# Kernel tuning notes

Measured on AMD Instinct MI355X. Metric: run time of the kernel, lower is better.

The kernel has to match this reference:

```python
import jax, jax.numpy as jnp
import numpy as np

IN_SIZE = 224
KERNEL = 5
STRIDE = 1
IN_CH = 16
OUT_CH = 64
LAMB = 5.0
LR = 0.005
GAMMA = 0.99
EPS_ = 0.01
NH = (IN_SIZE - KERNEL) // STRIDE + 1          # 220 output positions per side
NB_TILES = NH * NH                              # 48400 tiles


def setup_inputs() -> dict:
    key = jax.random.key(0)
    k1, k2 = jax.random.split(key)
    x = jax.random.normal(k1, (1, IN_CH, IN_SIZE, IN_SIZE), dtype=jnp.float32)
    # torch.nn.init.uniform_(param, a=0, b=1)
    W = jax.random.uniform(k2, (OUT_CH, IN_CH, KERNEL, KERNEL), dtype=jnp.float32)
    exp_avg = jnp.zeros((OUT_CH,), dtype=jnp.float32)
    return {"x": x, "W": W, "exp_avg": exp_avg, "clamped": 0}


def _inhibition(out):
    out = jax.nn.relu(out)
    m = jnp.max(out, axis=1, keepdims=True)     # max over channel dim
    out = out / (m + 1e-9)
    return out ** LAMB


def _flatten_input(x):
    # mirrors x.unfold(2,k,s).unfold(3,k,s) -> [T, C*k*k] with (C, kh, kw) ordering
    starts = jnp.arange(NH) * STRIDE
    rows = starts[:, None] + jnp.arange(KERNEL)  # [NH, K]
    p = x[0][:, rows]                            # [C, NH, K, W]
    p = p[:, :, :, rows]                         # [C, NH, K, NH, K]
    p = p.transpose(1, 3, 0, 2, 4)               # [NH, NH, C, K, K]
    return p.reshape(NB_TILES, -1)               # [T, D]


def reference(x, W, exp_avg, clamped):
    # forward conv + inhibition
    out = jax.lax.conv_general_dilated(
        x, W, (STRIDE, STRIDE), 'VALID',
        dimension_numbers=('NCHW', 'OIHW', 'NCHW'))
    out = _inhibition(out)                       # [1, O, NH, NH]

    # Hebbian FullyOrthogonal update (no-grad buffer update in the original)
    y = out[0].transpose(1, 2, 0).reshape(-1, OUT_CH)   # [T, O]
    xf = _flatten_input(x)                               # [T, D]
    Wf = W.reshape(OUT_CH, -1)                           # [O, D]
    # mean_t( lr * (y_t (x) x_t - y_t (x) (y_t W)) ) = lr/T * (Y^T X - (Y^T Y) W)
    yty = y.T @ y                                        # [O, O]
    avg_delta = (LR / NB_TILES) * (y.T @ xf - yty @ Wf)  # [O, D]
    Wnew = jax.nn.relu(Wf + avg_delta).reshape(OUT_CH, IN_CH, KERNEL, KERNEL)
    exp_new = GAMMA * exp_avg + (1.0 - GAMMA) * jnp.mean(y, axis=0)

    # weight decay scaling
    A = exp_new / jnp.mean(exp_new)
    gfp = EPS_ * jnp.tanh(-EPS_ * (A - 1.0)) + 1.0
    gfn = 1.0 / gfp
    pos = jnp.where(Wnew > 0, Wnew, 0.0) * gfp.reshape(-1, 1, 1, 1)
    neg = jnp.where(Wnew < 0, Wnew, 0.0) * gfn.reshape(-1, 1, 1, 1)
    Wfinal = pos + neg
    return out, Wfinal, exp_new
```

## Files before the change

### kernel.cpp

```cpp
#include <hip/hip_runtime.h>
#include <stdint.h>

#define IN_SIZE 224
#define KER 5
#define IN_CH 16
#define OUT_CH 64
#define NH 220
#define NB_TILES (NH * NH)
#define XCH (IN_SIZE * IN_SIZE)
#define OUT_PLANE NB_TILES
#define KP2 51200
#define XS 52224
#define LR_OVER_NB ((float)(0.005 / 48400.0))
#define GAMMA_F 0.99f
#define ONE_MINUS_GAMMA 0.01f
#define EPS_F 0.01f

#define NCHUNK 64
#define CK 800
#define PSTRIDE (64 * 512)

typedef __attribute__((ext_vector_type(8))) short short8;
typedef __attribute__((ext_vector_type(4))) float floatx4;

__device__ inline uint16_t f2bf(float f) {
    uint32_t u = __float_as_uint(f);
    return (uint16_t)((u + 0x7FFFu + ((u >> 16) & 1u)) >> 16);
}
__device__ inline float bf2f(uint16_t h) { return __uint_as_float((uint32_t)h << 16); }

__global__ __launch_bounds__(256) void prepa_kernel(const float* __restrict__ W,
                                                    uint16_t* __restrict__ wrh,
                                                    uint16_t* __restrict__ wrl) {
    int idx = blockIdx.x * 256 + threadIdx.x;
    if (idx >= 13 * 4 * 64 * 8) return;
    int j = idx & 7;
    int lane = (idx >> 3) & 63;
    int ocg = (idx >> 9) & 3;
    int t = idx >> 11;
    int k = (lane >> 4) * 8 + j;
    int s = k >> 4, c = k & 15;
    int oc = 16 * ocg + (lane & 15);
    int tap = 2 * t + s;
    float v = (tap < 25) ? W[oc * 400 + c * 25 + tap] : 0.f;
    uint16_t h = f2bf(v);
    wrh[idx] = h;
    wrl[idx] = f2bf(v - bf2f(h));
}

__global__ __launch_bounds__(256) void conv_prep_kernel(const uint16_t* __restrict__ wrh,
                                                        const uint16_t* __restrict__ wrl,
                                                        float* __restrict__ out,
                                                        uint16_t* __restrict__ yb,
                                                        const float* __restrict__ x,
                                                        uint16_t* __restrict__ xs,
                                                        uint16_t* __restrict__ ones) {
    if (blockIdx.x >= 770) {
        int t = (blockIdx.x - 770) * 256 + threadIdx.x;
        const int perq = XS / 4;
        if (t < 5 * 16 * perq) {
            int kj = t / (16 * perq);
            int rem = t - kj * (16 * perq);
            int c = rem / perq;
            int q = (rem - c * perq) * 4;
            int base = c * XCH;
            ushort4 o;
            int i0 = q + kj;     o.x = f2bf(x[base + (i0 < XCH ? i0 : XCH - 1)]);
            int i1 = q + kj + 1; o.y = f2bf(x[base + (i1 < XCH ? i1 : XCH - 1)]);
            int i2 = q + kj + 2; o.z = f2bf(x[base + (i2 < XCH ? i2 : XCH - 1)]);
            int i3 = q + kj + 3; o.w = f2bf(x[base + (i3 < XCH ? i3 : XCH - 1)]);
            *(ushort4*)(xs + (kj * 16 + c) * XS + q) = o;
        }
        ushort4 z = {0, 0, 0, 0};
        if (t < 64 * 480) {
            int r = t / 480, q = (t - r * 480) * 4;
            *(ushort4*)(yb + r * KP2 + 49280 + q) = z;
        }
        if (t < 64 * 220) {
            int o = t / 220, i = t - o * 220;
            *(ushort4*)(yb + o * KP2 + i * 224 + 220) = z;
        }
        if (t < 12816) {
            ushort4 o1 = {0x3F80, 0x3F80, 0x3F80, 0x3F80};
            ((ushort4*)ones)[t] = o1;
        }
        return;
    }

    const int lane = threadIdx.x & 63;
    const int w = threadIdx.x >> 6;
    const int l15 = lane & 15;
    const int quad = lane >> 4;
    const int P0 = blockIdx.x * 64;
    const int chalf = quad & 1;
    const int sq = quad >> 1;

    __shared__ uint16_t bsh[5 * 68 * 16];
    __shared__ uint16_t bsl[5 * 68 * 16];
    for (int u = threadIdx.x; u < 680; u += 256) {
        int row = u >> 1;
        int half = u & 1;
        int strip = row / 68;
        int rr = row - strip * 68;
        int grow = P0 + strip * 224 + rr;
        bool inb = grow < XCH;
        uint32_t dh[4], dl[4];
#pragma unroll
        for (int q = 0; q < 4; q++) {
            float v0 = inb ? x[(half * 8 + 2 * q) * XCH + grow] : 0.f;
            float v1 = inb ? x[(half * 8 + 2 * q + 1) * XCH + grow] : 0.f;
            uint16_t h0 = f2bf(v0), h1 = f2bf(v1);
            uint16_t l0 = f2bf(v0 - bf2f(h0)), l1 = f2bf(v1 - bf2f(h1));
            dh[q] = (uint32_t)h0 | ((uint32_t)h1 << 16);
            dl[q] = (uint32_t)l0 | ((uint32_t)l1 << 16);
        }
        int swz = (u ^ ((row >> 2) & 1)) * 8;
        *(uint4*)(bsh + swz) = make_uint4(dh[0], dh[1], dh[2], dh[3]);
        *(uint4*)(bsl + swz) = make_uint4(dl[0], dl[1], dl[2], dl[3]);
    }
    __syncthreads();

    floatx4 acc[4];
#pragma unroll
    for (int g = 0; g < 4; g++) acc[g] = (floatx4){0.f, 0.f, 0.f, 0.f};

#pragma unroll
    for (int t = 0; t < 13; t++) {
        short8 ah = *(const short8*)(wrh + ((t * 4 + w) * 64 + lane) * 8);
        short8 al = *(const short8*)(wrl + ((t * 4 + w) * 64 + lane) * 8);
        const int tap0 = 2 * t, tap1 = 2 * t + 1;
        const int ki0 = tap0 / 5, kj0 = tap0 % 5;
        const int ki1 = (tap1 <= 24) ? tap1 / 5 : 0;
        const int kj1 = (tap1 <= 24) ? tap1 % 5 : 0;
        const int strip = sq ? ki1 : ki0;
        const int kjv = sq ? kj1 : kj0;
#pragma unroll
        for (int g = 0; g < 4; g++) {
            int lrow = strip * 68 + 16 * g + l15 + kjv;
            int unit = lrow * 2 + chalf;
            int off = (unit ^ ((lrow >> 2) & 1)) * 8;
            short8 bh = *(const short8*)(bsh + off);
            short8 bl = *(const short8*)(bsl + off);
            acc[g] = __builtin_amdgcn_mfma_f32_16x16x32_bf16(ah, bh, acc[g], 0, 0, 0);
            acc[g] = __builtin_amdgcn_mfma_f32_16x16x32_bf16(ah, bl, acc[g], 0, 0, 0);
            acc[g] = __builtin_amdgcn_mfma_f32_16x16x32_bf16(al, bh, acc[g], 0, 0, 0);
        }
    }

    __shared__ float wmax[4][64];
    float pmax[4];
#pragma unroll
    for (int g = 0; g < 4; g++) {
        float mx = fmaxf(fmaxf(acc[g][0], acc[g][1]), fmaxf(acc[g][2], acc[g][3]));
        mx = fmaxf(mx, 0.f);
        mx = fmaxf(mx, __shfl_xor(mx, 16));
        mx = fmaxf(mx, __shfl_xor(mx, 32));
        pmax[g] = mx;
    }
    if (quad == 0) {
#pragma unroll
        for (int g = 0; g < 4; g++) wmax[w][g * 16 + l15] = pmax[g];
    }
    __syncthreads();

#pragma unroll
    for (int g = 0; g < 4; g++) {
        int P = P0 + 16 * g + l15;
        int i = P / 224;
        int j = P - i * 224;
        bool valid = j < NH;
        float mx = fmaxf(fmaxf(wmax[0][g * 16 + l15], wmax[1][g * 16 + l15]),
                         fmaxf(wmax[2][g * 16 + l15], wmax[3][g * 16 + l15]));
        float inv = 1.f / (mx + 1e-9f);
#pragma unroll
        for (int r = 0; r < 4; r++) {
            float tv = fmaxf(acc[g][r], 0.f) * inv;
            float t2 = tv * tv;
            tv = t2 * t2 * tv;
            if (valid) {
                int oc = 16 * w + quad * 4 + r;
                out[oc * OUT_PLANE + i * NH + j] = tv;
                yb[oc * KP2 + P] = f2bf(tv);
            }
        }
    }
}

__global__ __launch_bounds__(256) void gemm_kernel(const uint16_t* __restrict__ yb,
                                                   const uint16_t* __restrict__ xs,
                                                   const uint16_t* __restrict__ ones,
                                                   float* __restrict__ Mpart) {
    __shared__ uint16_t As[2][64 * 40];
    __shared__ uint16_t Bs[2][64 * 40];
    const int tid = threadIdx.x;
    const int lane = tid & 63;
    const int w = tid >> 6;
    const int l15 = lane & 15;
    const int quad = lane >> 4;
    const int kg = quad * 8;
    const int b = blockIdx.x;
    const int xcd = b & 7;
    const int t8 = b >> 3;
    const int ntile = t8 & 7;
    const int chunk = xcd + 8 * (t8 >> 3);
    const int k0 = chunk * CK;

    const int sr = tid >> 2;
    const int sseg = (tid & 3) * 8;
    const uint16_t* pa = yb + sr * KP2 + k0 + sseg;

    int n_g = ntile * 64 + sr;
    const uint16_t* pbase;
    if (n_g < 400) {
        int c = n_g / 25;
        int r = n_g - 25 * c;
        int ki = r / 5;
        int kj = r - 5 * ki;
        pbase = xs + (kj * 16 + c) * XS + ki * 224;
    } else if (n_g < 464) {
        pbase = yb + (n_g - 400) * KP2;
    } else if (n_g == 464) {
        pbase = ones;
    } else {
        pbase = yb;
    }
    const uint16_t* pb = pbase + k0 + sseg;

    floatx4 acc[4];
#pragma unroll
    for (int i = 0; i < 4; i++) acc[i] = (floatx4){0.f, 0.f, 0.f, 0.f};

    uint4 ra = *(const uint4*)pa;
    uint4 rb = *(const uint4*)pb;

    for (int s = 0; s < 25; s++) {
        const int p = s & 1;
        *(uint4*)&As[p][sr * 40 + sseg] = ra;
        *(uint4*)&Bs[p][sr * 40 + sseg] = rb;
        __syncthreads();
        if (s + 1 < 25) {
            pa += 32;
            pb += 32;
            ra = *(const uint4*)pa;
            rb = *(const uint4*)pb;
        }
        short8 af = *(const short8*)&As[p][(16 * w + l15) * 40 + kg];
#pragma unroll
        for (int ng = 0; ng < 4; ng++) {
            short8 bf = *(const short8*)&Bs[p][(16 * ng + l15) * 40 + kg];
            acc[ng] = __builtin_amdgcn_mfma_f32_16x16x32_bf16(af, bf, acc[ng], 0, 0, 0);
        }
        __syncthreads();
    }

    float* dst = Mpart + chunk * PSTRIDE;
#pragma unroll
    for (int ng = 0; ng < 4; ng++) {
        int col = ntile * 64 + ng * 16 + l15;
        if (col < 465) {
#pragma unroll
            for (int r = 0; r < 4; r++)
                dst[(16 * w + quad * 4 + r) * 512 + col] = acc[ng][r];
        }
    }
}

__global__ __launch_bounds__(256) void finalize_w_kernel(const float* __restrict__ W,
                                                         const float* __restrict__ Mpart,
                                                         const float* __restrict__ exp_avg,
                                                         float* __restrict__ Wout,
                                                         float* __restrict__ expout) {
    __shared__ float gfps[OUT_CH];
    __shared__ float ytys[2][OUT_CH];
    const int tid = threadIdx.x;
    const int bid = blockIdx.x;
    const int first_o = (bid * 256) / 400;

    if (tid < OUT_CH) {
        int o = tid;
        float cs = 0.f;
#pragma unroll 8
        for (int ch = 0; ch < NCHUNK; ch++) cs += Mpart[ch * PSTRIDE + o * 512 + 464];
        float e = GAMMA_F * exp_avg[o] + ONE_MINUS_GAMMA * (cs / (float)NB_TILES);
        float s = e;
        for (int off = 32; off; off >>= 1) s += __shfl_down(s, off);
        s = __shfl(s, 0);
        float A = e / (s / (float)OUT_CH);
        gfps[o] = EPS_F * tanhf(-EPS_F * (A - 1.f)) + 1.f;
        if (bid == 0) expout[o] = e;
    }
    if (tid >= 128) {
        int t = tid - 128;
        int orow = first_o + (t >> 6);
        int k = t & 63;
        float s = 0.f;
        if (orow < OUT_CH) {
#pragma unroll 8
            for (int ch = 0; ch < NCHUNK; ch++) s += Mpart[ch * PSTRIDE + orow * 512 + 400 + k];
        }
        ytys[t >> 6][k] = s;
    }
    __syncthreads();

    int idx = bid * 256 + tid;
    int o = idx / 400;
    int q = idx - o * 400;
    float Mv = 0.f;
#pragma unroll 8
    for (int ch = 0; ch < NCHUNK; ch++) Mv += Mpart[ch * PSTRIDE + o * 512 + q];
    const float* yrow = ytys[o - first_o];
    float dot = 0.f;
#pragma unroll 8
    for (int k = 0; k < OUT_CH; k++) dot = fmaf(yrow[k], W[k * 400 + q], dot);
    float wv = W[idx] + LR_OVER_NB * (Mv - dot);
    wv = fmaxf(wv, 0.f);
    float gp = gfps[o];
    float pos = (wv > 0.f ? wv : 0.f) * gp;
    float neg = (wv < 0.f ? wv : 0.f) / gp;
    Wout[idx] = pos + neg;
}

extern "C" void kernel_launch(void* const* d_in, const int* in_sizes, int n_in,
                              void* d_out, int out_size, void* d_ws, size_t ws_size,
                              hipStream_t stream) {
    const float* x = (const float*)d_in[0];
    const float* W = (const float*)d_in[1];
    const float* exp_avg = (const float*)d_in[2];
    float* out = (float*)d_out;

    float* wsf = (float*)d_ws;
    float* Mpart = wsf + 29760;
    uint16_t* wrh = (uint16_t*)Mpart;
    uint16_t* wrl = wrh + 26624;
    uint16_t* ybf = (uint16_t*)(wsf + 29760 + NCHUNK * PSTRIDE);
    uint16_t* xsb = ybf + OUT_CH * KP2;
    uint16_t* ones = xsb + 5 * 16 * XS;

    float* Wout = out + OUT_CH * OUT_PLANE;
    float* expout = Wout + OUT_CH * IN_CH * KER * KER;

    prepa_kernel<<<104, 256, 0, stream>>>(W, wrh, wrl);
    conv_prep_kernel<<<770 + 4080, 256, 0, stream>>>(wrh, wrl, out, ybf, x, xsb, ones);
    gemm_kernel<<<512, 256, 0, stream>>>(ybf, xsb, ones, Mpart);
    finalize_w_kernel<<<100, 256, 0, stream>>>(W, Mpart, exp_avg, Wout, expout);
}
```

Baseline: 110.1 us.

## Fuse finalize into GEMM via atomic grid barrier; widen x bf16 conversion

```diff
diff --git a/kernel.cpp b/kernel.cpp
--- a/kernel.cpp
+++ b/kernel.cpp
@@ -31,7 +31,9 @@
 
 __global__ __launch_bounds__(256) void prepa_kernel(const float* __restrict__ W,
                                                     uint16_t* __restrict__ wrh,
-                                                    uint16_t* __restrict__ wrl) {
+                                                    uint16_t* __restrict__ wrl,
+                                                    unsigned* __restrict__ cnt) {
+    if (blockIdx.x == 0 && threadIdx.x == 0) *cnt = 0u;
     int idx = blockIdx.x * 256 + threadIdx.x;
     if (idx >= 13 * 4 * 64 * 8) return;
     int j = idx & 7;
@@ -57,19 +59,23 @@
                                                         uint16_t* __restrict__ ones) {
     if (blockIdx.x >= 770) {
         int t = (blockIdx.x - 770) * 256 + threadIdx.x;
-        const int perq = XS / 4;
-        if (t < 5 * 16 * perq) {
-            int kj = t / (16 * perq);
-            int rem = t - kj * (16 * perq);
-            int c = rem / perq;
-            int q = (rem - c * perq) * 4;
+        const int perq8 = XS / 8;
+        {
+            int kj = t / (16 * perq8);
+            int rem = t - kj * (16 * perq8);
+            int c = rem / perq8;
+            int q = (rem - c * perq8) * 8;
             int base = c * XCH;
-            ushort4 o;
-            int i0 = q + kj;     o.x = f2bf(x[base + (i0 < XCH ? i0 : XCH - 1)]);
-            int i1 = q + kj + 1; o.y = f2bf(x[base + (i1 < XCH ? i1 : XCH - 1)]);
-            int i2 = q + kj + 2; o.z = f2bf(x[base + (i2 < XCH ? i2 : XCH - 1)]);
-            int i3 = q + kj + 3; o.w = f2bf(x[base + (i3 < XCH ? i3 : XCH - 1)]);
-            *(ushort4*)(xs + (kj * 16 + c) * XS + q) = o;
+            uint32_t d[4];
+#pragma unroll
+            for (int p = 0; p < 4; p++) {
+                int i0 = q + kj + 2 * p;
+                int i1 = i0 + 1;
+                uint16_t h0 = f2bf(x[base + (i0 < XCH ? i0 : XCH - 1)]);
+                uint16_t h1 = f2bf(x[base + (i1 < XCH ? i1 : XCH - 1)]);
+                d[p] = (uint32_t)h0 | ((uint32_t)h1 << 16);
+            }
+            *(uint4*)(xs + (kj * 16 + c) * XS + q) = make_uint4(d[0], d[1], d[2], d[3]);
         }
         ushort4 z = {0, 0, 0, 0};
         if (t < 64 * 480) {
@@ -186,10 +192,15 @@
     }
 }
 
-__global__ __launch_bounds__(256) void gemm_kernel(const uint16_t* __restrict__ yb,
-                                                   const uint16_t* __restrict__ xs,
-                                                   const uint16_t* __restrict__ ones,
-                                                   float* __restrict__ Mpart) {
+__global__ __launch_bounds__(256) void gemm_fin_kernel(const uint16_t* __restrict__ yb,
+                                                       const uint16_t* __restrict__ xs,
+                                                       const uint16_t* __restrict__ ones,
+                                                       float* __restrict__ Mpart,
+                                                       unsigned* __restrict__ cnt,
+                                                       const float* __restrict__ W,
+                                                       const float* __restrict__ exp_avg,
+                                                       float* __restrict__ Wout,
+                                                       float* __restrict__ expout) {
     __shared__ uint16_t As[2][64 * 40];
     __shared__ uint16_t Bs[2][64 * 40];
     const int tid = threadIdx.x;
@@ -263,17 +274,21 @@
                 dst[(16 * w + quad * 4 + r) * 512 + col] = acc[ng][r];
         }
     }
-}
-
-__global__ __launch_bounds__(256) void finalize_w_kernel(const float* __restrict__ W,
-                                                         const float* __restrict__ Mpart,
-                                                         const float* __restrict__ exp_avg,
-                                                         float* __restrict__ Wout,
-                                                         float* __restrict__ expout) {
+
+    __syncthreads();
+    __threadfence();
+    if (tid == 0) atomicAdd(cnt, 1u);
+    if (b >= 100) return;
+    if (tid == 0) {
+        while (__hip_atomic_load(cnt, __ATOMIC_ACQUIRE, __HIP_MEMORY_SCOPE_AGENT) < 512u)
+            __builtin_amdgcn_s_sleep(2);
+    }
+    __syncthreads();
+    __threadfence();
+
     __shared__ float gfps[OUT_CH];
     __shared__ float ytys[2][OUT_CH];
-    const int tid = threadIdx.x;
-    const int bid = blockIdx.x;
+    const int bid = b;
     const int first_o = (bid * 256) / 400;
 
     if (tid < OUT_CH) {
@@ -329,6 +344,7 @@
     float* out = (float*)d_out;
 
     float* wsf = (float*)d_ws;
+    unsigned* cnt = (unsigned*)wsf;
     float* Mpart = wsf + 29760;
     uint16_t* wrh = (uint16_t*)Mpart;
     uint16_t* wrl = wrh + 26624;
@@ -339,8 +355,7 @@
     float* Wout = out + OUT_CH * OUT_PLANE;
     float* expout = Wout + OUT_CH * IN_CH * KER * KER;
 
-    prepa_kernel<<<104, 256, 0, stream>>>(W, wrh, wrl);
-    conv_prep_kernel<<<770 + 4080, 256, 0, stream>>>(wrh, wrl, out, ybf, x, xsb, ones);
-    gemm_kernel<<<512, 256, 0, stream>>>(ybf, xsb, ones, Mpart);
-    finalize_w_kernel<<<100, 256, 0, stream>>>(W, Mpart, exp_avg, Wout, expout);
-}
+    prepa_kernel<<<104, 256, 0, stream>>>(W, wrh, wrl, cnt);
+    conv_prep_kernel<<<770 + 2040, 256, 0, stream>>>(wrh, wrl, out, ybf, x, xsb, ones);
+    gemm_fin_kernel<<<512, 256, 0, stream>>>(ybf, xsb, ones, Mpart, cnt, W, exp_avg, Wout, expout);
+}
```

Result: slower. 191.7 us (+74.1%).
